# Performance work log

Hardware: AMD Instinct MI355X
Metric: run time of the kernel (lower is better)

Reference implementation:

```python
import jax, jax.numpy as jnp
import numpy as np

NUM_HEADS = 12


def setup_inputs() -> dict:
    key = jax.random.key(0)
    ks = jax.random.split(key, 10)
    B, N, C = 8, 1024, 768
    H = NUM_HEADS
    return {
        "x": jax.random.normal(ks[0], (B, N, C), dtype=jnp.float32),
        "geometric": jax.random.uniform(ks[1], (B, 1, 1, 1), dtype=jnp.float32),
        "text": jax.random.uniform(ks[2], (B, 1, 1, 1), dtype=jnp.float32),
        "color": jax.random.uniform(ks[3], (B, 1, 1, 1), dtype=jnp.float32),
        "W_qkv": jax.random.normal(ks[4], (C, 3 * C), dtype=jnp.float32) * 0.02,
        "W_proj": jax.random.normal(ks[5], (C, C), dtype=jnp.float32) * 0.02,
        "b_proj": jax.random.normal(ks[6], (C,), dtype=jnp.float32) * 0.02,
        "geo_bias": jax.random.normal(ks[7], (1, H, 1, 1), dtype=jnp.float32) * 0.1,
        "txt_bias": jax.random.normal(ks[8], (1, H, 1, 1), dtype=jnp.float32) * 0.1,
        "col_bias": jax.random.normal(ks[9], (1, H, 1, 1), dtype=jnp.float32) * 0.1,
    }


def reference(x, geometric, text, color, W_qkv, W_proj, b_proj, geo_bias, txt_bias, col_bias):
    B, N, C = x.shape
    H = NUM_HEADS
    Dh = C // H
    scale = Dh ** -0.5
    # qkv: [B, N, 3, H, Dh] -> q,k,v each [B, H, N, Dh]
    qkv = (x @ W_qkv).reshape(B, N, 3, H, Dh)
    q = jnp.transpose(qkv[:, :, 0], (0, 2, 1, 3))
    k = jnp.transpose(qkv[:, :, 1], (0, 2, 1, 3))
    v = jnp.transpose(qkv[:, :, 2], (0, 2, 1, 3))
    # scores [B, H, N, N] with additive per-head logo biases
    attn = jnp.einsum("bhnd,bhmd->bhnm", q, k) * scale
    attn = attn + geo_bias * geometric + txt_bias * text + col_bias * color
    attn = jax.nn.softmax(attn, axis=-1)
    out = jnp.einsum("bhnm,bhmd->bhnd", attn, v)  # [B, H, N, Dh]
    out = jnp.transpose(out, (0, 2, 1, 3)).reshape(B, N, C)
    return out @ W_proj + b_proj
```

## Files before the change

kernel.cpp:

```cpp
#include <hip/hip_runtime.h>
#include <hip/hip_bf16.h>


typedef __bf16 b16x8 __attribute__((ext_vector_type(8)));
typedef float f32x4 __attribute__((ext_vector_type(4)));

__device__ __forceinline__ ushort f2b(float f) {
    union { float f; uint u; } v; v.f = f;
    uint u = v.u;
    u += 0x7fffu + ((u >> 16) & 1u);
    return (ushort)(u >> 16);
}

__device__ __forceinline__ uint packbf(float a, float b) {
    union { float f; uint u; } ua, ub; ua.f = a; ub.f = b;
    return ((ua.u + 0x8000u) >> 16) | ((ub.u + 0x8000u) & 0xffff0000u);
}

__device__ __forceinline__ void async_cp16(const void* g, void* l) {
    __builtin_amdgcn_global_load_lds(
        (const __attribute__((address_space(1))) unsigned int*)g,
        (__attribute__((address_space(3))) unsigned int*)l, 16, 0, 0);
}


__global__ __launch_bounds__(256)
void k_prep(const float* __restrict__ x, ushort* __restrict__ xb,
            const float* __restrict__ Wqkv, ushort* __restrict__ wqkvt,
            const float* __restrict__ Wproj, ushort* __restrict__ wprojt) {
    __shared__ ushort T[64][65];
    const int blk = blockIdx.x;
    const int t   = threadIdx.x;

    if (blk < 6144) {
        const int i = blk * 256 + t;
        const float4 v = reinterpret_cast<const float4*>(x)[i];
        ushort4 o;
        o.x = f2b(v.x); o.y = f2b(v.y); o.z = f2b(v.z); o.w = f2b(v.w);
        reinterpret_cast<ushort4*>(xb)[i] = o;
        return;
    }

    const bool isqkv = (blk < 6576);
    const int idx = isqkv ? (blk - 6144) : (blk - 6576);
    const int Nin = isqkv ? 2304 : 768;
    const float* W  = isqkv ? Wqkv : Wproj;
    ushort* Wt      = isqkv ? wqkvt : wprojt;
    const int k0 = (idx % 12) * 64;
    const int n0 = (idx / 12) * 64;
    const int r  = t >> 4, cg = (t & 15) * 4;
    #pragma unroll
    for (int rr = 0; rr < 64; rr += 16) {
        const float4 v = *reinterpret_cast<const float4*>(&W[(size_t)(k0 + r + rr) * Nin + n0 + cg]);
        T[r + rr][cg + 0] = f2b(v.x); T[r + rr][cg + 1] = f2b(v.y);
        T[r + rr][cg + 2] = f2b(v.z); T[r + rr][cg + 3] = f2b(v.w);
    }
    __syncthreads();
    #pragma unroll
    for (int rr = 0; rr < 64; rr += 16) {
        ushort4 o;
        o.x = T[cg + 0][r + rr]; o.y = T[cg + 1][r + rr];
        o.z = T[cg + 2][r + rr]; o.w = T[cg + 3][r + rr];
        *reinterpret_cast<ushort4*>(&Wt[(size_t)(n0 + r + rr) * 768 + k0 + cg]) = o;
    }
}


template<int MODE>
__global__ __launch_bounds__(256, 2)
void k_gemm(const ushort* __restrict__ A, const ushort* __restrict__ Bt,
            ushort* __restrict__ qo, ushort* __restrict__ ko, ushort* __restrict__ vo,
            float* __restrict__ co, const float* __restrict__ bias,
            int M, int N, int K) {
    __shared__ ushort As[2][128 * 32];
    __shared__ ushort Bs[2][128 * 32];
    const int id   = blockIdx.x;
    const int xcd  = id & 7;
    const int s    = id >> 3;
    const int by   = xcd * 8 + (s & 7);
    const int bx   = s >> 3;
    const int tid  = threadIdx.x;
    const int lane = tid & 63;
    const int w    = tid >> 6;
    const int wm   = w >> 1, wn = w & 1;
    const int m16  = lane & 15, quad = lane >> 4;
    const int mbase = by * 128, nbase = bx * 128;

    f32x4 acc[4][4];
    #pragma unroll
    for (int i = 0; i < 4; i++)
        #pragma unroll
        for (int j = 0; j < 4; j++) acc[i][j] = (f32x4){0.f, 0.f, 0.f, 0.f};

    const int rS = w * 32 + (lane >> 2);
    const int cS = (lane & 3) * 8;
    const int wOff0 = (w * 2 + 0) * 512;
    const int wOff1 = (w * 2 + 1) * 512;
    const ushort* gA0 = &A [(size_t)(mbase + rS)      * K + cS];
    const ushort* gA1 = &A [(size_t)(mbase + rS + 16) * K + cS];
    const ushort* gB0 = &Bt[(size_t)(nbase + rS)      * K + cS];
    const ushort* gB1 = &Bt[(size_t)(nbase + rS + 16) * K + cS];

    async_cp16(gA0, &As[0][wOff0]);
    async_cp16(gA1, &As[0][wOff1]);
    async_cp16(gB0, &Bs[0][wOff0]);
    async_cp16(gB1, &Bs[0][wOff1]);

    for (int kt = 0; kt < K; kt += 32) {
        const int cur = (kt >> 5) & 1, nxt = cur ^ 1;
        __syncthreads();
        if (kt + 32 < K) {
            async_cp16(gA0 + kt + 32, &As[nxt][wOff0]);
            async_cp16(gA1 + kt + 32, &As[nxt][wOff1]);
            async_cp16(gB0 + kt + 32, &Bs[nxt][wOff0]);
            async_cp16(gB1 + kt + 32, &Bs[nxt][wOff1]);
        }

        b16x8 af[4], bf[4];
        #pragma unroll
        for (int i = 0; i < 4; i++)
            af[i] = *reinterpret_cast<const b16x8*>(&As[cur][(wm * 64 + i * 16 + m16) * 32 + quad * 8]);
        #pragma unroll
        for (int j = 0; j < 4; j++)
            bf[j] = *reinterpret_cast<const b16x8*>(&Bs[cur][(wn * 64 + j * 16 + m16) * 32 + quad * 8]);
        #pragma unroll
        for (int i = 0; i < 4; i++)
            #pragma unroll
            for (int j = 0; j < 4; j++)
                acc[i][j] = __builtin_amdgcn_mfma_f32_16x16x32_bf16(bf[j], af[i], acc[i][j], 0, 0, 0);
    }

    #pragma unroll
    for (int j = 0; j < 4; j++) {
        const int f0 = nbase + wn * 64 + j * 16 + quad * 4;
        #pragma unroll
        for (int i = 0; i < 4; i++) {
            const int tok = mbase + wm * 64 + i * 16 + m16;
            const int b = tok >> 10, n = tok & 1023;
            if (MODE == 0) {
                const int sp  = f0 / 768;
                const int rem = f0 - sp * 768;
                const int h   = rem >> 6;
                const int d0  = rem & 63;
                if (sp < 2) {
                    ushort4 pk;
                    pk.x = f2b(acc[i][j][0]); pk.y = f2b(acc[i][j][1]);
                    pk.z = f2b(acc[i][j][2]); pk.w = f2b(acc[i][j][3]);
                    ushort* base = (sp == 0) ? qo : ko;
                    *reinterpret_cast<ushort4*>(
                        &base[((size_t)(b * 12 + h) * 1024 + n) * 64 + d0]) = pk;
                } else {
                    #pragma unroll
                    for (int r = 0; r < 4; r++)
                        vo[((size_t)(b * 12 + h) * 64 + d0 + r) * 1024 + n] =
                            f2b(acc[i][j][r]);
                }
            } else {
                float4 val;
                val.x = acc[i][j][0] + bias[f0 + 0];
                val.y = acc[i][j][1] + bias[f0 + 1];
                val.z = acc[i][j][2] + bias[f0 + 2];
                val.w = acc[i][j][3] + bias[f0 + 3];
                *reinterpret_cast<float4*>(&co[(size_t)tok * N + f0]) = val;
            }
        }
    }
}


#define AP 72

__global__ __launch_bounds__(256)
void k_attn(const ushort* __restrict__ qa, const ushort* __restrict__ ka,
            const ushort* __restrict__ vt, ushort* __restrict__ ao) {
    __shared__ ushort Ks[64 * AP];
    __shared__ ushort Vs[64 * AP];

    const int l    = blockIdx.x;
    const int xcd  = l & 7;
    const int g    = l >> 3;
    const int head = (g % 12) * 8 + xcd;
    const int qsup = g / 12;
    const int tid  = threadIdx.x;
    const int w    = tid >> 6;
    const int lane = tid & 63;
    const int n    = lane & 15;
    const int q    = lane >> 4;

    const ushort* qh = qa + (size_t)head * 65536;
    const ushort* kh = ka + (size_t)head * 65536;
    const ushort* vh = vt + (size_t)head * 65536;
    const int qrow0 = qsup * 128 + w * 32;

    b16x8 bq0[2], bq1[2];
    #pragma unroll
    for (int u = 0; u < 2; u++) {
        bq0[u] = *reinterpret_cast<const b16x8*>(&qh[(qrow0 + u * 16 + n) * 64 + q * 8]);
        bq1[u] = *reinterpret_cast<const b16x8*>(&qh[(qrow0 + u * 16 + n) * 64 + 32 + q * 8]);
    }

    const int kr0 = tid >> 3, kc0 = (tid & 7) * 8;
    const int kr1 = kr0 + 32, kc1 = kc0;

    int4 kg0, kg1, vg0, vg1;
    kg0 = *reinterpret_cast<const int4*>(&kh[(0 + kr0) * 64 + kc0]);
    kg1 = *reinterpret_cast<const int4*>(&kh[(0 + kr1) * 64 + kc1]);
    vg0 = *reinterpret_cast<const int4*>(&vh[kr0 * 1024 + 0 + kc0]);
    vg1 = *reinterpret_cast<const int4*>(&vh[kr1 * 1024 + 0 + kc1]);

    f32x4 o[2][4];
    #pragma unroll
    for (int u = 0; u < 2; u++)
        #pragma unroll
        for (int dt = 0; dt < 4; dt++) o[u][dt] = (f32x4){0, 0, 0, 0};
    float Lacc[2] = {0.f, 0.f};

    const float SC = 0.125f * 1.4426950408889634f;
    const int s0 = ((q & 1) * 2) * 16 + n;
    const int s1 = s0 + 16;
    const bool lowq = (q < 2);

    for (int m0 = 0; m0 < 1024; m0 += 64) {
        *reinterpret_cast<int4*>(&Ks[kr0 * AP + kc0]) = kg0;
        *reinterpret_cast<int4*>(&Ks[kr1 * AP + kc1]) = kg1;
        *reinterpret_cast<int4*>(&Vs[kr0 * AP + kc0]) = vg0;
        *reinterpret_cast<int4*>(&Vs[kr1 * AP + kc1]) = vg1;
        __syncthreads();

        if (m0 + 64 < 1024) {
            kg0 = *reinterpret_cast<const int4*>(&kh[(m0 + 64 + kr0) * 64 + kc0]);
            kg1 = *reinterpret_cast<const int4*>(&kh[(m0 + 64 + kr1) * 64 + kc1]);
            vg0 = *reinterpret_cast<const int4*>(&vh[kr0 * 1024 + m0 + 64 + kc0]);
            vg1 = *reinterpret_cast<const int4*>(&vh[kr1 * 1024 + m0 + 64 + kc1]);
        }

        #pragma unroll
        for (int mc = 0; mc < 2; mc++) {
            b16x8 ka0t[2], ka1t[2];
            #pragma unroll
            for (int t = 0; t < 2; t++) {
                ka0t[t] = *reinterpret_cast<const b16x8*>(&Ks[(mc * 32 + t * 16 + n) * AP + q * 8]);
                ka1t[t] = *reinterpret_cast<const b16x8*>(&Ks[(mc * 32 + t * 16 + n) * AP + 32 + q * 8]);
            }
            f32x4 st[2][2];
            #pragma unroll
            for (int u = 0; u < 2; u++)
                #pragma unroll
                for (int t = 0; t < 2; t++) {
                    st[u][t] = (f32x4){0, 0, 0, 0};
                    st[u][t] = __builtin_amdgcn_mfma_f32_16x16x32_bf16(ka0t[t], bq0[u], st[u][t], 0, 0, 0);
                    st[u][t] = __builtin_amdgcn_mfma_f32_16x16x32_bf16(ka1t[t], bq1[u], st[u][t], 0, 0, 0);
                }

            union { uint4 u4; b16x8 v; } bp[2];
            #pragma unroll
            for (int u = 0; u < 2; u++) {
                float p00 = __builtin_amdgcn_exp2f(st[u][0][0] * SC);
                float p01 = __builtin_amdgcn_exp2f(st[u][0][1] * SC);
                float p02 = __builtin_amdgcn_exp2f(st[u][0][2] * SC);
                float p03 = __builtin_amdgcn_exp2f(st[u][0][3] * SC);
                float p10 = __builtin_amdgcn_exp2f(st[u][1][0] * SC);
                float p11 = __builtin_amdgcn_exp2f(st[u][1][1] * SC);
                float p12 = __builtin_amdgcn_exp2f(st[u][1][2] * SC);
                float p13 = __builtin_amdgcn_exp2f(st[u][1][3] * SC);
                Lacc[u] += ((p00 + p01) + (p02 + p03)) + ((p10 + p11) + (p12 + p13));

                const uint pk00 = packbf(p00, p01), pk01 = packbf(p02, p03);
                const uint pk10 = packbf(p10, p11), pk11 = packbf(p12, p13);

                uint a, b, dw0, dw1, dw2, dw3;
                a = __shfl((int)pk00, s0); b = __shfl((int)pk10, s0); dw0 = lowq ? a : b;
                a = __shfl((int)pk01, s0); b = __shfl((int)pk11, s0); dw1 = lowq ? a : b;
                a = __shfl((int)pk00, s1); b = __shfl((int)pk10, s1); dw2 = lowq ? a : b;
                a = __shfl((int)pk01, s1); b = __shfl((int)pk11, s1); dw3 = lowq ? a : b;
                bp[u].u4 = (uint4){dw0, dw1, dw2, dw3};
            }

            #pragma unroll
            for (int dt = 0; dt < 4; dt++) {
                const b16x8 av = *reinterpret_cast<const b16x8*>(
                    &Vs[(dt * 16 + n) * AP + mc * 32 + q * 8]);
                #pragma unroll
                for (int u = 0; u < 2; u++)
                    o[u][dt] = __builtin_amdgcn_mfma_f32_16x16x32_bf16(av, bp[u].v, o[u][dt], 0, 0, 0);
            }
        }
        __syncthreads();
    }

    const int bb = head / 12, h = head - bb * 12;
    #pragma unroll
    for (int u = 0; u < 2; u++) {
        float L = Lacc[u];
        L += __shfl_xor(L, 16);
        L += __shfl_xor(L, 32);
        const float inv = 1.f / L;
        ushort* dst = ao + ((size_t)(bb * 1024 + qrow0 + u * 16 + n)) * 768 + h * 64 + q * 4;
        #pragma unroll
        for (int dt = 0; dt < 4; dt++) {
            ushort4 pk;
            pk.x = f2b(o[u][dt][0] * inv);
            pk.y = f2b(o[u][dt][1] * inv);
            pk.z = f2b(o[u][dt][2] * inv);
            pk.w = f2b(o[u][dt][3] * inv);
            *reinterpret_cast<ushort4*>(dst + dt * 16) = pk;
        }
    }
}


extern "C" void kernel_launch(void* const* d_in, const int* in_sizes, int n_in,
                              void* d_out, int out_size, void* d_ws, size_t ws_size,
                              hipStream_t stream) {
    (void)in_sizes; (void)n_in; (void)out_size; (void)ws_size;
    const float* x     = (const float*)d_in[0];
    const float* Wqkv  = (const float*)d_in[4];
    const float* Wproj = (const float*)d_in[5];
    const float* bproj = (const float*)d_in[6];
    float* out = (float*)d_out;

    char* ws = (char*)d_ws;
    ushort* xb     = (ushort*)ws; ws += (size_t)8192 * 768 * 2;
    ushort* wqkvt  = (ushort*)ws; ws += (size_t)2304 * 768 * 2;
    ushort* wprojt = (ushort*)ws; ws += (size_t)768  * 768 * 2;
    ushort* qa     = (ushort*)ws; ws += (size_t)96 * 1024 * 64 * 2;
    ushort* ka     = (ushort*)ws; ws += (size_t)96 * 1024 * 64 * 2;
    ushort* vt     = (ushort*)ws; ws += (size_t)96 * 64 * 1024 * 2;
    ushort* ao     = (ushort*)ws; ws += (size_t)8192 * 768 * 2;

    k_prep<<<dim3(6720), dim3(256), 0, stream>>>(x, xb, Wqkv, wqkvt, Wproj, wprojt);
    k_gemm<0><<<dim3(1152), dim3(256), 0, stream>>>(xb, wqkvt, qa, ka, vt,
                                                    nullptr, nullptr, 8192, 2304, 768);
    k_attn<<<dim3(768), dim3(256), 0, stream>>>(qa, ka, vt, ao);
    k_gemm<1><<<dim3(384), dim3(256), 0, stream>>>(ao, wprojt, nullptr, nullptr, nullptr,
                                                   out, bproj, 8192, 768, 768);
}
```

Measured before the change: 212.4 us.

## Replace QKV GEMM with 256x288-tile, 512-thread kernel using fine-grained pipelining

The fused QKV projection moves to a dedicated kernel with 256x288 output tiles, 8 waves and about 136KB of dynamic LDS. Loads are split into half-K stages with explicit vmcnt waits, raw barriers and setprio around the MFMA blocks, so global-to-LDS copies overlap with compute. For the V columns the MFMA operand order is swapped, which gives a transposed accumulator and lets V be written to its transposed layout as vector stores instead of scalar ones. The grid drops to 256 blocks, one per CU, which risks lower occupancy and a tail imbalance in exchange for more data reuse per tile.

```diff
diff --git a/kernel.cpp b/kernel.cpp
--- a/kernel.cpp
+++ b/kernel.cpp
@@ -66,12 +66,148 @@
 }
 
 
-template<int MODE>
+#define SBAR()   asm volatile("s_barrier" ::: "memory")
+#define WAITV(n) asm volatile("s_waitcnt vmcnt(" #n ")" ::: "memory")
+
+#define LDSA(buf, kh, ii) (*reinterpret_cast<const b16x8*>( \
+    &lds[(buf) * 16384 + (kh) * 8192 + (wm * 64 + (ii) * 16 + m16) * 32 + q8]))
+#define LDSB(buf, kh, jj) (*reinterpret_cast<const b16x8*>( \
+    &lds[32768 + (buf) * 18432 + (kh) * 9216 + (wn * 144 + (jj) * 16 + m16) * 32 + q8]))
+
+#define STA(bufn, ktv, kh) { \
+    async_cp16(&A[(size_t)(mbase + (2*w)*16 + srow) * 768 + (ktv) + (kh)*32 + ssub], \
+               &lds[(bufn)*16384 + (kh)*8192 + (2*w)*512]); \
+    async_cp16(&A[(size_t)(mbase + (2*w+1)*16 + srow) * 768 + (ktv) + (kh)*32 + ssub], \
+               &lds[(bufn)*16384 + (kh)*8192 + (2*w+1)*512]); }
+#define STB(bufn, ktv, kh) { \
+    async_cp16(&Bt[(size_t)(nbase + (2*w)*16 + srow) * 768 + (ktv) + (kh)*32 + ssub], \
+               &lds[32768 + (bufn)*18432 + (kh)*9216 + (2*w)*512]); \
+    async_cp16(&Bt[(size_t)(nbase + (2*w+1)*16 + srow) * 768 + (ktv) + (kh)*32 + ssub], \
+               &lds[32768 + (bufn)*18432 + (kh)*9216 + (2*w+1)*512]); \
+    if (w < 2) { \
+        async_cp16(&Bt[(size_t)(nbase + (16+w)*16 + srow) * 768 + (ktv) + (kh)*32 + ssub], \
+                   &lds[32768 + (bufn)*18432 + (kh)*9216 + (16+w)*512]); } }
+
+#define PAIR(I0, kh, bufc) { \
+    const b16x8 a0 = LDSA(bufc, kh, I0), a1 = LDSA(bufc, kh, (I0) + 1); \
+    _Pragma("unroll") \
+    for (int j = 0; j < 9; j++) { \
+        if (colbase + j * 16 >= 1536) { \
+            acc[I0][j]     = __builtin_amdgcn_mfma_f32_16x16x32_bf16(a0, bf[j], acc[I0][j], 0, 0, 0); \
+            acc[(I0)+1][j] = __builtin_amdgcn_mfma_f32_16x16x32_bf16(a1, bf[j], acc[(I0)+1][j], 0, 0, 0); \
+        } else { \
+            acc[I0][j]     = __builtin_amdgcn_mfma_f32_16x16x32_bf16(bf[j], a0, acc[I0][j], 0, 0, 0); \
+            acc[(I0)+1][j] = __builtin_amdgcn_mfma_f32_16x16x32_bf16(bf[j], a1, acc[(I0)+1][j], 0, 0, 0); \
+        } } }
+
+__global__ __launch_bounds__(512, 2)
+void k_qkv(const ushort* __restrict__ A, const ushort* __restrict__ Bt,
+           ushort* __restrict__ qo, ushort* __restrict__ ko,
+           ushort* __restrict__ vo) {
+    extern __shared__ ushort lds[];
+    const int id   = blockIdx.x;
+    const int bx   = id & 7;
+    const int by   = id >> 3;
+    const int tid  = threadIdx.x;
+    const int w    = tid >> 6;
+    const int lane = tid & 63;
+    const int wm   = w >> 1, wn = w & 1;
+    const int m16  = lane & 15, q8 = (lane >> 4) * 8;
+    const int mbase = by * 256, nbase = bx * 288;
+    const int colbase = nbase + wn * 144;
+    const int srow = lane >> 2, ssub = (lane & 3) * 8;
+
+    f32x4 acc[4][9];
+    #pragma unroll
+    for (int i = 0; i < 4; i++)
+        #pragma unroll
+        for (int j = 0; j < 9; j++) acc[i][j] = (f32x4){0.f, 0.f, 0.f, 0.f};
+
+    STA(0, 0, 0); STB(0, 0, 0);
+    STA(0, 0, 1); STB(0, 0, 1);
+    if (w < 2) { WAITV(5); } else { WAITV(4); }
+    SBAR();
+
+    b16x8 bf[9];
+    int cur = 0;
+    for (int t = 0; t < 12; t++) {
+        const int kt  = t * 64;
+        const int nxt = cur ^ 1;
+        const bool more = (t < 11);
+        #pragma unroll
+        for (int j = 0; j < 9; j++) bf[j] = LDSB(cur, 0, j);
+        if (more) STA(nxt, kt + 64, 0);
+        __builtin_amdgcn_s_setprio(1);
+        PAIR(0, 0, cur);
+        __builtin_amdgcn_s_setprio(0);
+        SBAR();
+        if (more) STB(nxt, kt + 64, 0);
+        __builtin_amdgcn_s_setprio(1);
+        PAIR(2, 0, cur);
+        __builtin_amdgcn_s_setprio(0);
+        if (more) { if (w < 2) { WAITV(5); } else { WAITV(4); } }
+        else      { WAITV(0); }
+        SBAR();
+        #pragma unroll
+        for (int j = 0; j < 9; j++) bf[j] = LDSB(cur, 1, j);
+        if (more) STA(nxt, kt + 64, 1);
+        __builtin_amdgcn_s_setprio(1);
+        PAIR(0, 1, cur);
+        __builtin_amdgcn_s_setprio(0);
+        SBAR();
+        if (more) STB(nxt, kt + 64, 1);
+        __builtin_amdgcn_s_setprio(1);
+        PAIR(2, 1, cur);
+        __builtin_amdgcn_s_setprio(0);
+        if (more) {
+            if (w < 2) { WAITV(5); } else { WAITV(4); }
+            SBAR();
+        }
+        cur = nxt;
+    }
+
+    #pragma unroll
+    for (int j = 0; j < 9; j++) {
+        const int col16 = colbase + j * 16;
+        if (col16 < 1536) {
+            const int f0  = col16 + (q8 >> 1);
+            const int sp  = (f0 >= 768) ? 1 : 0;
+            const int rem = f0 - sp * 768;
+            const int h   = rem >> 6, d0 = rem & 63;
+            ushort* base  = sp ? ko : qo;
+            #pragma unroll
+            for (int i = 0; i < 4; i++) {
+                const int tok = mbase + wm * 64 + i * 16 + m16;
+                const int b = tok >> 10, n = tok & 1023;
+                ushort4 pk;
+                pk.x = f2b(acc[i][j][0]); pk.y = f2b(acc[i][j][1]);
+                pk.z = f2b(acc[i][j][2]); pk.w = f2b(acc[i][j][3]);
+                *reinterpret_cast<ushort4*>(
+                    &base[((size_t)(b * 12 + h) * 1024 + n) * 64 + d0]) = pk;
+            }
+        } else {
+            const int f   = col16 + m16;
+            const int rem = f - 1536;
+            const int h   = rem >> 6, d0 = rem & 63;
+            #pragma unroll
+            for (int i = 0; i < 4; i++) {
+                const int tok0 = mbase + wm * 64 + i * 16 + (q8 >> 1);
+                const int b = tok0 >> 10, n0 = tok0 & 1023;
+                ushort4 pk;
+                pk.x = f2b(acc[i][j][0]); pk.y = f2b(acc[i][j][1]);
+                pk.z = f2b(acc[i][j][2]); pk.w = f2b(acc[i][j][3]);
+                *reinterpret_cast<ushort4*>(
+                    &vo[((size_t)(b * 12 + h) * 64 + d0) * 1024 + n0]) = pk;
+            }
+        }
+    }
+}
+
+
 __global__ __launch_bounds__(256, 2)
-void k_gemm(const ushort* __restrict__ A, const ushort* __restrict__ Bt,
-            ushort* __restrict__ qo, ushort* __restrict__ ko, ushort* __restrict__ vo,
+void k_proj(const ushort* __restrict__ A, const ushort* __restrict__ Bt,
             float* __restrict__ co, const float* __restrict__ bias,
-            int M, int N, int K) {
+            int N, int K) {
     __shared__ ushort As[2][128 * 32];
     __shared__ ushort Bs[2][128 * 32];
     const int id   = blockIdx.x;
@@ -115,19 +251,18 @@
             async_cp16(gB0 + kt + 32, &Bs[nxt][wOff0]);
             async_cp16(gB1 + kt + 32, &Bs[nxt][wOff1]);
         }
-
-        b16x8 af[4], bf[4];
+        b16x8 af[4], bfr[4];
         #pragma unroll
         for (int i = 0; i < 4; i++)
             af[i] = *reinterpret_cast<const b16x8*>(&As[cur][(wm * 64 + i * 16 + m16) * 32 + quad * 8]);
         #pragma unroll
         for (int j = 0; j < 4; j++)
-            bf[j] = *reinterpret_cast<const b16x8*>(&Bs[cur][(wn * 64 + j * 16 + m16) * 32 + quad * 8]);
+            bfr[j] = *reinterpret_cast<const b16x8*>(&Bs[cur][(wn * 64 + j * 16 + m16) * 32 + quad * 8]);
         #pragma unroll
         for (int i = 0; i < 4; i++)
             #pragma unroll
             for (int j = 0; j < 4; j++)
-                acc[i][j] = __builtin_amdgcn_mfma_f32_16x16x32_bf16(bf[j], af[i], acc[i][j], 0, 0, 0);
+                acc[i][j] = __builtin_amdgcn_mfma_f32_16x16x32_bf16(bfr[j], af[i], acc[i][j], 0, 0, 0);
     }
 
     #pragma unroll
@@ -136,33 +271,12 @@
         #pragma unroll
         for (int i = 0; i < 4; i++) {
             const int tok = mbase + wm * 64 + i * 16 + m16;
-            const int b = tok >> 10, n = tok & 1023;
-            if (MODE == 0) {
-                const int sp  = f0 / 768;
-                const int rem = f0 - sp * 768;
-                const int h   = rem >> 6;
-                const int d0  = rem & 63;
-                if (sp < 2) {
-                    ushort4 pk;
-                    pk.x = f2b(acc[i][j][0]); pk.y = f2b(acc[i][j][1]);
-                    pk.z = f2b(acc[i][j][2]); pk.w = f2b(acc[i][j][3]);
-                    ushort* base = (sp == 0) ? qo : ko;
-                    *reinterpret_cast<ushort4*>(
-                        &base[((size_t)(b * 12 + h) * 1024 + n) * 64 + d0]) = pk;
-                } else {
-                    #pragma unroll
-                    for (int r = 0; r < 4; r++)
-                        vo[((size_t)(b * 12 + h) * 64 + d0 + r) * 1024 + n] =
-                            f2b(acc[i][j][r]);
-                }
-            } else {
-                float4 val;
-                val.x = acc[i][j][0] + bias[f0 + 0];
-                val.y = acc[i][j][1] + bias[f0 + 1];
-                val.z = acc[i][j][2] + bias[f0 + 2];
-                val.w = acc[i][j][3] + bias[f0 + 3];
-                *reinterpret_cast<float4*>(&co[(size_t)tok * N + f0]) = val;
-            }
+            float4 val;
+            val.x = acc[i][j][0] + bias[f0 + 0];
+            val.y = acc[i][j][1] + bias[f0 + 1];
+            val.z = acc[i][j][2] + bias[f0 + 2];
+            val.w = acc[i][j][3] + bias[f0 + 3];
+            *reinterpret_cast<float4*>(&co[(size_t)tok * N + f0]) = val;
         }
     }
 }
@@ -328,10 +442,15 @@
     ushort* vt     = (ushort*)ws; ws += (size_t)96 * 64 * 1024 * 2;
     ushort* ao     = (ushort*)ws; ws += (size_t)8192 * 768 * 2;
 
+    static int attr_set = 0;
+    if (!attr_set) {
+        hipFuncSetAttribute((const void*)k_qkv,
+                            hipFuncAttributeMaxDynamicSharedMemorySize, 139264);
+        attr_set = 1;
+    }
+
     k_prep<<<dim3(6720), dim3(256), 0, stream>>>(x, xb, Wqkv, wqkvt, Wproj, wprojt);
-    k_gemm<0><<<dim3(1152), dim3(256), 0, stream>>>(xb, wqkvt, qa, ka, vt,
-                                                    nullptr, nullptr, 8192, 2304, 768);
+    k_qkv<<<dim3(256), dim3(512), 139264, stream>>>(xb, wqkvt, qa, ka, vt);
     k_attn<<<dim3(768), dim3(256), 0, stream>>>(qa, ka, vt, ao);
-    k_gemm<1><<<dim3(384), dim3(256), 0, stream>>>(ao, wprojt, nullptr, nullptr, nullptr,
-                                                   out, bproj, 8192, 768, 768);
-}
+    k_proj<<<dim3(384), dim3(256), 0, stream>>>(ao, wprojt, out, bproj, 768, 768);
+}
```

New measurement: 386.2 us. 81.9% more time.
